# Optimization experiments

Measured on AMD Instinct MI355X. Metric: run time of the kernel, lower is better.

The kernel has to match this reference:

```python
import jax, jax.numpy as jnp
import numpy as np

N = 100000   # nodes
H = 96       # hidden_dim
A = 32       # attn_dim
De = 16      # edge_embeddings_dim
E = 500000   # edges per edge type
NEG_SLOPE = 0.01  # torch F.leaky_relu default


def setup_inputs() -> dict:
    key = jax.random.key(0)
    ks = jax.random.split(key, 24)
    nrm = lambda k, shape, s=1.0: jax.random.normal(k, shape, dtype=jnp.float32) * s
    idx = lambda k: jax.random.randint(k, (E,), 0, N, dtype=jnp.int32)
    Din = 2 * H + De
    return {
        'h': nrm(ks[0], (N, H)),
        'src0': idx(ks[1]), 'dst0': idx(ks[2]),
        'src1': idx(ks[3]), 'dst1': idx(ks[4]),
        'src2': idx(ks[5]), 'dst2': idx(ks[6]),
        'Wm0': nrm(ks[7], (Din, H), Din ** -0.5), 'bm0': jnp.zeros((H,), jnp.float32), 'ef0': nrm(ks[8], (De,)),
        'Wm1': nrm(ks[9], (Din, H), Din ** -0.5), 'bm1': jnp.zeros((H,), jnp.float32), 'ef1': nrm(ks[10], (De,)),
        'Wm2': nrm(ks[11], (Din, H), Din ** -0.5), 'bm2': jnp.zeros((H,), jnp.float32), 'ef2': nrm(ks[12], (De,)),
        'Wn0': nrm(ks[13], (H, A), H ** -0.5), 'Wa0': nrm(ks[14], (2 * A, 1), (2 * A) ** -0.5),
        'Wn1': nrm(ks[15], (H, A), H ** -0.5), 'Wa1': nrm(ks[16], (2 * A, 1), (2 * A) ** -0.5),
        'Wu': nrm(ks[17], (4 * H, H), (4 * H) ** -0.5), 'bu': jnp.zeros((H,), jnp.float32),
    }


def _leaky(x):
    return jnp.where(x > 0, x, NEG_SLOPE * x)


def _edge_msg(h, src, dst, Wm, bm, ef):
    # cat(src_h, dst_h, edge_feature) -> Linear  (dropout p=0, eval mode)
    x = jnp.concatenate([h[src], h[dst], jnp.broadcast_to(ef, (src.shape[0], ef.shape[0]))], axis=-1)
    return x @ Wm + bm  # [E, H]


def _mean_agg(m, dst):
    # fn.mean('m','msg'): per-destination mean over incoming edges
    s = jax.ops.segment_sum(m, dst, num_segments=N)
    c = jax.ops.segment_sum(jnp.ones((m.shape[0],), m.dtype), dst, num_segments=N)
    return s / jnp.maximum(c, 1.0)[:, None]


def _attn_agg(scores, m, dst):
    # per-destination softmax over mailbox (variable-size), then weighted sum
    smax = jax.ops.segment_max(scores, dst, num_segments=N)
    ex = jnp.exp(scores - smax[dst])
    den = jax.ops.segment_sum(ex, dst, num_segments=N)
    num = jax.ops.segment_sum(ex[:, None] * m, dst, num_segments=N)
    return num / jnp.maximum(den, 1e-9)[:, None]


def reference(h, src0, dst0, src1, dst1, src2, dst2,
              Wm0, bm0, ef0, Wm1, bm1, ef1, Wm2, bm2, ef2,
              Wn0, Wa0, Wn1, Wa1, Wu, bu):
    # edge type 0: intra_diff (attention), type 1: inter_diff (attention), type 2: intra_lt (mean)
    m0 = _edge_msg(h, src0, dst0, Wm0, bm0, ef0)
    m1 = _edge_msg(h, src1, dst1, Wm1, bm1, ef1)
    m2 = _edge_msg(h, src2, dst2, Wm2, bm2, ef2)

    z0 = h @ Wn0  # [N, A]
    s0 = _leaky(jnp.concatenate([z0[src0], z0[dst0]], axis=-1) @ Wa0)[:, 0]  # [E]
    z1 = h @ Wn1
    s1 = _leaky(jnp.concatenate([z1[src1], z1[dst1]], axis=-1) @ Wa1)[:, 0]

    msg0 = _attn_agg(s0, m0, dst0)   # [N, H]
    msg1 = _attn_agg(s1, m1, dst1)
    msg2 = _mean_agg(m2, dst2)

    # cross_reducer='stack' then concat over edge-type dim -> [N, 3H]
    mcat = jnp.concatenate([msg0, msg1, msg2], axis=-1)
    # cell node update: Linear(cat(h, m)) + ReLU
    return jax.nn.relu(jnp.concatenate([h, mcat], axis=-1) @ Wu + bu)
```

## Files before the change

### kernel.cpp

```cpp
#include <hip/hip_runtime.h>
#include <hip/hip_bf16.h>
#include <cstdint>

#define NN 100000
#define HH 96
#define AD 32
#define DE 16
#define EE 500000
#define NEG 0.01f

#define GSH 10
#define GSZ 1024
#define KB 98
#define CH 4096
#define BPT 123
#define PCAP 801056

typedef __bf16 bf16x8 __attribute__((ext_vector_type(8)));
typedef float  f32x4  __attribute__((ext_vector_type(4)));
typedef unsigned long long ull;
typedef unsigned long long ull2 __attribute__((ext_vector_type(2)));

__device__ __forceinline__ unsigned short f2b(float x) {
    union { float f; unsigned int u; } v; v.f = x;
    unsigned int r = v.u + 0x7fffu + ((v.u >> 16) & 1u);
    return (unsigned short)(r >> 16);
}
__device__ __forceinline__ float b2f(unsigned short h) {
    union { unsigned int u; float f; } v; v.u = ((unsigned int)h) << 16;
    return v.f;
}

__global__ void prep_kernel(const float* Wm0, const float* bm0, const float* ef0,
                            const float* Wm1, const float* bm1, const float* ef1,
                            const float* Wm2, const float* bm2, const float* ef2,
                            const float* Wn0, const float* Wa0,
                            const float* Wn1, const float* Wa1,
                            const float* Wu,
                            float* cvec, float* wvec,
                            unsigned short* BfN, unsigned short* BfU) {
    const float* Wm[3] = {Wm0, Wm1, Wm2};
    const float* bm[3] = {bm0, bm1, bm2};
    const float* ef[3] = {ef0, ef1, ef2};
    const int total = 288 + 384 + 55296 + 36864;
    for (int i = blockIdx.x * blockDim.x + threadIdx.x; i < total;
         i += gridDim.x * blockDim.x) {
        if (i < 288) {
            int t = i / 96, j = i % 96;
            float s = bm[t][j];
            for (int k = 0; k < DE; ++k) s += ef[t][k] * Wm[t][(2 * HH + k) * HH + j];
            cvec[i] = s;
        } else if (i < 288 + 384) {
            int ii = i - 288;
            int kind = ii / 96, k = ii % 96;
            const float* Wn = (kind < 2) ? Wn0 : Wn1;
            const float* Wa = (kind < 2) ? Wa0 : Wa1;
            int off = (kind & 1) ? AD : 0;
            float s = 0.f;
            for (int a = 0; a < AD; ++a) s += Wn[k * AD + a] * Wa[off + a];
            wvec[ii] = s;
        } else if (i < 288 + 384 + 55296) {
            int ii = i - 672;
            int sec = ii / 9216; int rem = ii % 9216;
            int ksc = rem / 512; int lj = rem % 512;
            int ks = ksc / 6, c = ksc % 6;
            int lane = lj / 8, jj = lj % 8;
            int quad = lane / 16, m = lane % 16;
            int k = ks * 32 + quad * 8 + jj;
            int n = c * 16 + m;
            int mt = (sec < 3) ? sec : sec - 3;
            int rowoff = (sec < 3) ? 0 : HH;
            BfN[ii] = f2b(Wm[mt][(rowoff + k) * HH + n]);
        } else {
            int ii = i - (672 + 55296);
            int ksc = ii / 512; int lj = ii % 512;
            int ks = ksc / 6, c = ksc % 6;
            int lane = lj / 8, jj = lj % 8;
            int quad = lane / 16, m = lane % 16;
            int k = ks * 32 + quad * 8 + jj;
            int n = c * 16 + m;
            BfU[ii] = f2b(Wu[k * HH + n]);
        }
    }
}

__global__ void cast_uv_kernel(const float* __restrict__ h, const float* __restrict__ wvec,
                               unsigned short* __restrict__ hb, float* __restrict__ uv) {
    int lane = threadIdx.x & 31;
    int node = (blockIdx.x * blockDim.x + threadIdx.x) >> 5;
    if (node >= NN) return;
    float h0 = h[node * HH + lane];
    float h1 = h[node * HH + 32 + lane];
    float h2 = h[node * HH + 64 + lane];
    hb[node * HH + lane] = f2b(h0);
    hb[node * HH + 32 + lane] = f2b(h1);
    hb[node * HH + 64 + lane] = f2b(h2);
    float acc[4];
#pragma unroll
    for (int q = 0; q < 4; ++q)
        acc[q] = h0 * wvec[q * 96 + lane] + h1 * wvec[q * 96 + 32 + lane] +
                 h2 * wvec[q * 96 + 64 + lane];
#pragma unroll
    for (int d = 16; d >= 1; d >>= 1)
#pragma unroll
        for (int q = 0; q < 4; ++q) acc[q] += __shfl_down(acc[q], d, 32);
    if (lane == 0) {
#pragma unroll
        for (int q = 0; q < 4; ++q) uv[q * NN + node] = acc[q];
    }
}

__global__ void zero_kernel(float4* __restrict__ p, int n4) {
    for (int i = blockIdx.x * blockDim.x + threadIdx.x; i < n4;
         i += gridDim.x * blockDim.x)
        p[i] = make_float4(0.f, 0.f, 0.f, 0.f);
}

__global__ void bucket_hist(const int* __restrict__ d0, const int* __restrict__ d1,
                            const int* __restrict__ d2, int* __restrict__ bCnt) {
    __shared__ int hist[3 * KB];
    int t = threadIdx.x;
    for (int j = t; j < 3 * KB; j += 256) hist[j] = 0;
    __syncthreads();
    const int total = 3 * EE;
    for (int i = blockIdx.x * blockDim.x + t; i < total; i += gridDim.x * blockDim.x) {
        int ty = i / EE, e = i - ty * EE;
        const int* d = (ty == 0) ? d0 : (ty == 1) ? d1 : d2;
        atomicAdd(&hist[ty * KB + (d[e] >> GSH)], 1);
    }
    __syncthreads();
    for (int j = t; j < 3 * KB; j += 256)
        if (hist[j]) atomicAdd(&bCnt[j], hist[j]);
}

__global__ void bucket_scan(const int* __restrict__ bCnt, int* __restrict__ bBase,
                            int* __restrict__ gCursor) {
    __shared__ int hist[3 * KB];
    int t = threadIdx.x;
    if (t < 3 * KB) hist[t] = bCnt[t];
    __syncthreads();
    if (t < 3) {
        int run = 0;
        for (int b = 0; b < KB; ++b) {
            bBase[t * (KB + 1) + b] = run;
            gCursor[t * KB + b] = run;
            run += hist[t * KB + b];
        }
        bBase[t * (KB + 1) + KB] = run;
    }
}

__global__ __launch_bounds__(256) void bucket_scatter(
    const int* __restrict__ s0, const int* __restrict__ d0,
    const int* __restrict__ s1, const int* __restrict__ d1,
    const int* __restrict__ s2, const int* __restrict__ d2,
    int* __restrict__ gCursor, unsigned int* __restrict__ binned) {
    __shared__ unsigned int recs[CH];
    __shared__ unsigned short rnk[CH];
    __shared__ unsigned char bkt[CH];
    __shared__ int cnt[KB];
    __shared__ int gpos[KB];
    int t = threadIdx.x;
    int type = blockIdx.x / BPT;
    int chunk = (blockIdx.x % BPT) * CH;
    const int* src = (type == 0) ? s0 : (type == 1) ? s1 : s2;
    const int* dst = (type == 0) ? d0 : (type == 1) ? d1 : d2;
    if (t < KB) cnt[t] = 0;
    __syncthreads();
#pragma unroll
    for (int k = 0; k < CH / 256; ++k) {
        int idx = k * 256 + t;
        int e = chunk + idx;
        if (e < EE) {
            int s = src[e], d = dst[e];
            int b = d >> GSH;
            recs[idx] = ((unsigned int)s << GSH) | (unsigned int)(d & (GSZ - 1));
            bkt[idx] = (unsigned char)b;
            rnk[idx] = (unsigned short)atomicAdd(&cnt[b], 1);
        } else {
            bkt[idx] = 0xFF;
        }
    }
    __syncthreads();
    if (t < KB) {
        int c = cnt[t];
        gpos[t] = (c > 0) ? atomicAdd(&gCursor[type * KB + t], c) : 0;
    }
    __syncthreads();
    unsigned int* bout = binned + (size_t)type * EE;
#pragma unroll
    for (int k = 0; k < CH / 256; ++k) {
        int idx = k * 256 + t;
        unsigned char b = bkt[idx];
        if (b != 0xFF) bout[gpos[b] + rnk[idx]] = recs[idx];
    }
}

__global__ __launch_bounds__(256) void bucket_sort(
    const unsigned int* __restrict__ binned, const int* __restrict__ bBase,
    const float* __restrict__ uv,
    ull* __restrict__ rse, ull* __restrict__ wrec) {
    __shared__ int cnt[GSZ];
    __shared__ int tsum[256];
    __shared__ float vbuf[GSZ];
    int t = threadIdx.x;
    int type = blockIdx.x / KB;
    int b = blockIdx.x % KB;
    int nodeBase = b * GSZ;
    int eb = bBase[type * (KB + 1) + b];
    int en = bBase[type * (KB + 1) + b + 1];
    int n = en - eb;
    int pbase = eb + 3 * GSZ * b;
    const unsigned int* bin = binned + (size_t)type * EE + eb;
#pragma unroll
    for (int k = 0; k < GSZ / 256; ++k) cnt[k * 256 + t] = 0;
    if (type < 2) {
        const float* vsrc = uv + (2 * type + 1) * NN;
#pragma unroll
        for (int k = 0; k < GSZ / 256; ++k) {
            int nd = nodeBase + k * 256 + t;
            vbuf[k * 256 + t] = (nd < NN) ? vsrc[nd] : 0.f;
        }
    }
    __syncthreads();
    for (int i = t; i < n; i += 256) atomicAdd(&cnt[bin[i] & (GSZ - 1)], 1);
    __syncthreads();
    int v[4], pv[4], s = 0;
#pragma unroll
    for (int k = 0; k < 4; ++k) {
        v[k] = cnt[t * 4 + k];
        pv[k] = (v[k] + 3) & ~3;
        s += pv[k];
    }
    tsum[t] = s;
    __syncthreads();
    for (int off = 1; off < 256; off <<= 1) {
        int add = (t >= off) ? tsum[t - off] : 0;
        __syncthreads();
        tsum[t] += add;
        __syncthreads();
    }
    int run = tsum[t] - s;
    int offk[4];
#pragma unroll
    for (int k = 0; k < 4; ++k) { offk[k] = run; run += pv[k]; }
    ull* wb = wrec + (size_t)type * PCAP;
#pragma unroll
    for (int k = 0; k < 4; ++k) {
        int node = nodeBase + t * 4 + k;
        if (node < NN) {
            rse[(size_t)type * NN + node] =
                ((ull)(unsigned int)pv[k] << 32) | (unsigned int)(pbase + offk[k]);
            for (int q = v[k]; q < pv[k]; ++q) wb[pbase + offk[k] + q] = 0ull;
        }
    }
    __syncthreads();
#pragma unroll
    for (int k = 0; k < 4; ++k) cnt[t * 4 + k] = offk[k];
    __syncthreads();
    const float* usrc = uv + 2 * type * NN;
    for (int i = t; i < n; i += 256) {
        unsigned int r = bin[i];
        int dl = r & (GSZ - 1);
        int p = atomicAdd(&cnt[dl], 1);
        unsigned int sidx = r >> GSH;
        float w = 1.f;
        if (type < 2) {
            float c = usrc[sidx] + vbuf[dl];
            c = fmaxf(c, NEG * c);
            w = __expf(c);
        }
        wb[pbase + p] = ((ull)__float_as_uint(w) << 32) | (ull)(sidx * 192u);
    }
}

__global__ void aggregate_kernel(const ull* __restrict__ rse,
                                 const ull* __restrict__ wrec,
                                 const unsigned short* __restrict__ hb,
                                 unsigned short* __restrict__ hagg,
                                 float* __restrict__ den) {
    const size_t NH = (size_t)NN * HH;
    int lane = threadIdx.x & 31;
    int node = (blockIdx.x * blockDim.x + threadIdx.x) >> 5;
    if (node >= NN) return;
    int t = blockIdx.y;
    ull se = rse[(size_t)t * NN + node];
    int beg = (int)(unsigned int)se;
    int end = beg + (int)(se >> 32);
    const ull* wr = wrec + (size_t)t * PCAP;
    float a0 = 0.f, a1 = 0.f, a2 = 0.f, dn = 0.f;
    const char* b0 = (const char*)hb + 4 * lane;
    const char* b1 = (const char*)hb + 128 + 2 * lane;
#define EDGE(rec)                                                              \
    {                                                                          \
        float w = __uint_as_float((unsigned int)((rec) >> 32));                \
        unsigned int off = (unsigned int)(rec);                                \
        unsigned int dv = *(const unsigned int*)(b0 + off);                    \
        unsigned int sv = *(const unsigned short*)(b1 + off);                  \
        a0 += w * __uint_as_float(dv << 16);                                   \
        a1 += w * __uint_as_float(dv & 0xFFFF0000u);                           \
        a2 += w * __uint_as_float(sv << 16);                                   \
        dn += w;                                                               \
    }
    for (int j = beg; j < end; j += 4) {
        ull2 p0 = *(const ull2*)(wr + j);
        ull2 p1 = *(const ull2*)(wr + j + 2);
        EDGE(p0[0]);
        EDGE(p0[1]);
        EDGE(p1[0]);
        EDGE(p1[1]);
    }
#undef EDGE
    float inv = (dn > 0.f) ? 1.f / dn : 0.f;
    float q0 = a0 * inv, q1 = a1 * inv, q2 = a2 * inv;
    char* mr = (char*)(hagg + (size_t)t * NH + (size_t)node * HH);
    *(unsigned int*)(mr + 4 * lane) =
        (unsigned int)f2b(q0) | ((unsigned int)f2b(q1) << 16);
    *(unsigned short*)(mr + 128 + 2 * lane) = f2b(q2);
    if (lane == 0) den[(size_t)t * NN + node] = dn;
}

__global__ __launch_bounds__(256) void msg_gemm_kernel(const unsigned short* __restrict__ hagg,
                                                       const unsigned short* __restrict__ hb,
                                                       const unsigned short* __restrict__ BfN,
                                                       const float* __restrict__ den,
                                                       const float* __restrict__ cvec,
                                                       unsigned short* __restrict__ msgb) {
    const size_t NH = (size_t)NN * HH;
    int wave = threadIdx.x >> 6;
    int lane = threadIdx.x & 63;
    int quad = lane >> 4, m = lane & 15;
    int blk = blockIdx.x * 4 + wave;
    if (blk >= NN / 16) return;
    int t = blockIdx.y;
    int r0 = blk * 16;
    const unsigned short* ha = hagg + (size_t)t * NH;
    f32x4 acc[6] = {};
#pragma unroll
    for (int ks = 0; ks < 6; ++ks) {
        const unsigned short* ap =
            (ks < 3) ? ha + (size_t)(r0 + m) * HH + ks * 32 + quad * 8
                     : hb + (size_t)(r0 + m) * HH + (ks - 3) * 32 + quad * 8;
        int sec = (ks < 3) ? t : t + 3;
        int kk = (ks < 3) ? ks : ks - 3;
        bf16x8 af = *(const bf16x8*)ap;
#pragma unroll
        for (int c = 0; c < 6; ++c) {
            bf16x8 bfv = *(const bf16x8*)(BfN + (((sec * 3 + kk) * 6 + c) << 9) + lane * 8);
            acc[c] = __builtin_amdgcn_mfma_f32_16x16x32_bf16(af, bfv, acc[c], 0, 0, 0);
        }
    }
    float dn[4];
#pragma unroll
    for (int r = 0; r < 4; ++r) dn[r] = den[(size_t)t * NN + r0 + quad * 4 + r];
#pragma unroll
    for (int c = 0; c < 6; ++c) {
        float cv = cvec[t * 96 + c * 16 + m];
#pragma unroll
        for (int r = 0; r < 4; ++r) {
            int row = r0 + quad * 4 + r;
            float val = (dn[r] > 0.f) ? (acc[c][r] + cv) : 0.f;
            msgb[(size_t)row * 288 + t * 96 + c * 16 + m] = f2b(val);
        }
    }
}

__global__ __launch_bounds__(256) void update_gemm_kernel(const unsigned short* __restrict__ hb,
                                                          const unsigned short* __restrict__ msgb,
                                                          const unsigned short* __restrict__ BfU,
                                                          const float* __restrict__ bu,
                                                          float* __restrict__ out) {
    int wave = threadIdx.x >> 6;
    int lane = threadIdx.x & 63;
    int quad = lane >> 4, m = lane & 15;
    int blk = blockIdx.x * 4 + wave;
    if (blk >= NN / 16) return;
    int r0 = blk * 16;
    f32x4 acc[6] = {};
#pragma unroll
    for (int ks = 0; ks < 12; ++ks) {
        const unsigned short* ap =
            (ks < 3) ? hb + (size_t)(r0 + m) * HH + ks * 32 + quad * 8
                     : msgb + (size_t)(r0 + m) * 288 + (ks - 3) * 32 + quad * 8;
        bf16x8 af = *(const bf16x8*)ap;
#pragma unroll
        for (int c = 0; c < 6; ++c) {
            bf16x8 bfv = *(const bf16x8*)(BfU + ((ks * 6 + c) << 9) + lane * 8);
            acc[c] = __builtin_amdgcn_mfma_f32_16x16x32_bf16(af, bfv, acc[c], 0, 0, 0);
        }
    }
#pragma unroll
    for (int c = 0; c < 6; ++c) {
        float b = bu[c * 16 + m];
#pragma unroll
        for (int r = 0; r < 4; ++r) {
            int row = r0 + quad * 4 + r;
            float v2 = acc[c][r] + b;
            out[(size_t)row * HH + c * 16 + m] = v2 > 0.f ? v2 : 0.f;
        }
    }
}

extern "C" void kernel_launch(void* const* d_in, const int* in_sizes, int n_in,
                              void* d_out, int out_size, void* d_ws, size_t ws_size,
                              hipStream_t stream) {
    (void)in_sizes; (void)n_in; (void)out_size;
    const float* h   = (const float*)d_in[0];
    const int* srcs[3] = {(const int*)d_in[1], (const int*)d_in[3], (const int*)d_in[5]};
    const int* dsts[3] = {(const int*)d_in[2], (const int*)d_in[4], (const int*)d_in[6]};
    const float* Wm0 = (const float*)d_in[7];
    const float* bm0 = (const float*)d_in[8];
    const float* ef0 = (const float*)d_in[9];
    const float* Wm1 = (const float*)d_in[10];
    const float* bm1 = (const float*)d_in[11];
    const float* ef1 = (const float*)d_in[12];
    const float* Wm2 = (const float*)d_in[13];
    const float* bm2 = (const float*)d_in[14];
    const float* ef2 = (const float*)d_in[15];
    const float* Wn0 = (const float*)d_in[16];
    const float* Wa0 = (const float*)d_in[17];
    const float* Wn1 = (const float*)d_in[18];
    const float* Wa1 = (const float*)d_in[19];
    const float* Wu  = (const float*)d_in[20];
    const float* bu  = (const float*)d_in[21];
    float* out = (float*)d_out;

    const size_t NEED = 165016320;
    if (ws_size < NEED) return;
    char* w = (char*)d_ws;
    unsigned short* msgb    = (unsigned short*)(w + 0);
    unsigned short* hb      = (unsigned short*)(w + 57600000);
    unsigned short* hagg    = (unsigned short*)(w + 76800000);
    float*          den     = (float*)(w + 134400000);
    float*          uv      = (float*)(w + 135600000);
    float*          cvec    = (float*)(w + 137200000);
    float*          wvec    = (float*)(w + 137201280);
    unsigned short* BfN     = (unsigned short*)(w + 137202816);
    unsigned short* BfU     = (unsigned short*)(w + 137313408);
    int*            bBase   = (int*)(w + 137387136);
    int*            gCursor = (int*)(w + 137388416);
    int*            bCnt    = (int*)(w + 137389696);
    ull*            rse     = (ull*)(w + 137390976);
    unsigned int*   binned  = (unsigned int*)(w + 139790976);
    ull*            wrec    = (ull*)(w + 145790976);

    prep_kernel<<<128, 256, 0, stream>>>(Wm0, bm0, ef0, Wm1, bm1, ef1, Wm2, bm2, ef2,
                                         Wn0, Wa0, Wn1, Wa1, Wu, cvec, wvec, BfN, BfU);
    cast_uv_kernel<<<12500, 256, 0, stream>>>(h, wvec, hb, uv);

    zero_kernel<<<1, 256, 0, stream>>>((float4*)bCnt, 80);
    bucket_hist<<<512, 256, 0, stream>>>(dsts[0], dsts[1], dsts[2], bCnt);
    bucket_scan<<<1, 384, 0, stream>>>(bCnt, bBase, gCursor);
    bucket_scatter<<<3 * BPT, 256, 0, stream>>>(srcs[0], dsts[0], srcs[1], dsts[1],
                                                srcs[2], dsts[2], gCursor, binned);
    bucket_sort<<<3 * KB, 256, 0, stream>>>(binned, bBase, uv, rse, wrec);

    aggregate_kernel<<<dim3(12500, 3), 256, 0, stream>>>(rse, wrec, hb, hagg, den);
    msg_gemm_kernel<<<dim3(1563, 3), 256, 0, stream>>>(hagg, hb, BfN, den, cvec, msgb);
    update_gemm_kernel<<<1563, 256, 0, stream>>>(hb, msgb, BfU, bu, out);
}
```

Baseline: 331.2 us.

## Fuse message GEMM into update GEMM via per-wave LDS staging, drop zero kernel

The per-edge-type message GEMM and the node update GEMM become one kernel. Each wave computes the 16x96 message tile for each of the three edge types, stages it in LDS as bf16, and immediately accumulates it into the update output. This removes the global msgb intermediate (about 57 MB written and read back) and one launch. The bCnt zeroing moves into prep_kernel, removing another launch. In exchange the fused kernel has fewer blocks (no grid.y over types), serial work per wave, and no barrier around the per-wave LDS use, which relies on wave-local ordering.

Result: slower. 357.6 us (+8.0%).

```diff
diff --git a/kernel.cpp b/kernel.cpp
--- a/kernel.cpp
+++ b/kernel.cpp
@@ -38,13 +38,15 @@
                             const float* Wn1, const float* Wa1,
                             const float* Wu,
                             float* cvec, float* wvec,
-                            unsigned short* BfN, unsigned short* BfU) {
+                            unsigned short* BfN, unsigned short* BfU,
+                            int* bCnt) {
     const float* Wm[3] = {Wm0, Wm1, Wm2};
     const float* bm[3] = {bm0, bm1, bm2};
     const float* ef[3] = {ef0, ef1, ef2};
+    int tid0 = blockIdx.x * blockDim.x + threadIdx.x;
+    if (tid0 < 3 * KB) bCnt[tid0] = 0;
     const int total = 288 + 384 + 55296 + 36864;
-    for (int i = blockIdx.x * blockDim.x + threadIdx.x; i < total;
-         i += gridDim.x * blockDim.x) {
+    for (int i = tid0; i < total; i += gridDim.x * blockDim.x) {
         if (i < 288) {
             int t = i / 96, j = i % 96;
             float s = bm[t][j];
@@ -110,12 +112,6 @@
     }
 }
 
-__global__ void zero_kernel(float4* __restrict__ p, int n4) {
-    for (int i = blockIdx.x * blockDim.x + threadIdx.x; i < n4;
-         i += gridDim.x * blockDim.x)
-        p[i] = make_float4(0.f, 0.f, 0.f, 0.f);
-}
-
 __global__ void bucket_hist(const int* __restrict__ d0, const int* __restrict__ d1,
                             const int* __restrict__ d2, int* __restrict__ bCnt) {
     __shared__ int hist[3 * KB];
@@ -320,73 +316,74 @@
     if (lane == 0) den[(size_t)t * NN + node] = dn;
 }
 
-__global__ __launch_bounds__(256) void msg_gemm_kernel(const unsigned short* __restrict__ hagg,
-                                                       const unsigned short* __restrict__ hb,
-                                                       const unsigned short* __restrict__ BfN,
-                                                       const float* __restrict__ den,
-                                                       const float* __restrict__ cvec,
-                                                       unsigned short* __restrict__ msgb) {
+__global__ __launch_bounds__(256) void fused_gemm_kernel(
+    const unsigned short* __restrict__ hagg,
+    const unsigned short* __restrict__ hb,
+    const unsigned short* __restrict__ BfN,
+    const unsigned short* __restrict__ BfU,
+    const float* __restrict__ den,
+    const float* __restrict__ cvec,
+    const float* __restrict__ bu,
+    float* __restrict__ out) {
     const size_t NH = (size_t)NN * HH;
-    int wave = threadIdx.x >> 6;
-    int lane = threadIdx.x & 63;
-    int quad = lane >> 4, m = lane & 15;
-    int blk = blockIdx.x * 4 + wave;
-    if (blk >= NN / 16) return;
-    int t = blockIdx.y;
-    int r0 = blk * 16;
-    const unsigned short* ha = hagg + (size_t)t * NH;
-    f32x4 acc[6] = {};
-#pragma unroll
-    for (int ks = 0; ks < 6; ++ks) {
-        const unsigned short* ap =
-            (ks < 3) ? ha + (size_t)(r0 + m) * HH + ks * 32 + quad * 8
-                     : hb + (size_t)(r0 + m) * HH + (ks - 3) * 32 + quad * 8;
-        int sec = (ks < 3) ? t : t + 3;
-        int kk = (ks < 3) ? ks : ks - 3;
-        bf16x8 af = *(const bf16x8*)ap;
-#pragma unroll
-        for (int c = 0; c < 6; ++c) {
-            bf16x8 bfv = *(const bf16x8*)(BfN + (((sec * 3 + kk) * 6 + c) << 9) + lane * 8);
-            acc[c] = __builtin_amdgcn_mfma_f32_16x16x32_bf16(af, bfv, acc[c], 0, 0, 0);
-        }
-    }
-    float dn[4];
-#pragma unroll
-    for (int r = 0; r < 4; ++r) dn[r] = den[(size_t)t * NN + r0 + quad * 4 + r];
-#pragma unroll
-    for (int c = 0; c < 6; ++c) {
-        float cv = cvec[t * 96 + c * 16 + m];
-#pragma unroll
-        for (int r = 0; r < 4; ++r) {
-            int row = r0 + quad * 4 + r;
-            float val = (dn[r] > 0.f) ? (acc[c][r] + cv) : 0.f;
-            msgb[(size_t)row * 288 + t * 96 + c * 16 + m] = f2b(val);
-        }
-    }
-}
-
-__global__ __launch_bounds__(256) void update_gemm_kernel(const unsigned short* __restrict__ hb,
-                                                          const unsigned short* __restrict__ msgb,
-                                                          const unsigned short* __restrict__ BfU,
-                                                          const float* __restrict__ bu,
-                                                          float* __restrict__ out) {
+    __shared__ unsigned short lds[4][16][104];
     int wave = threadIdx.x >> 6;
     int lane = threadIdx.x & 63;
     int quad = lane >> 4, m = lane & 15;
     int blk = blockIdx.x * 4 + wave;
     if (blk >= NN / 16) return;
     int r0 = blk * 16;
-    f32x4 acc[6] = {};
-#pragma unroll
-    for (int ks = 0; ks < 12; ++ks) {
-        const unsigned short* ap =
-            (ks < 3) ? hb + (size_t)(r0 + m) * HH + ks * 32 + quad * 8
-                     : msgb + (size_t)(r0 + m) * 288 + (ks - 3) * 32 + quad * 8;
-        bf16x8 af = *(const bf16x8*)ap;
+    unsigned short (*L)[104] = lds[wave];
+
+    f32x4 accO[6] = {};
+#pragma unroll
+    for (int ks = 0; ks < 3; ++ks) {
+        bf16x8 af = *(const bf16x8*)(hb + (size_t)(r0 + m) * HH + ks * 32 + quad * 8);
 #pragma unroll
         for (int c = 0; c < 6; ++c) {
             bf16x8 bfv = *(const bf16x8*)(BfU + ((ks * 6 + c) << 9) + lane * 8);
-            acc[c] = __builtin_amdgcn_mfma_f32_16x16x32_bf16(af, bfv, acc[c], 0, 0, 0);
+            accO[c] = __builtin_amdgcn_mfma_f32_16x16x32_bf16(af, bfv, accO[c], 0, 0, 0);
+        }
+    }
+#pragma unroll 1
+    for (int t = 0; t < 3; ++t) {
+        const unsigned short* ha = hagg + (size_t)t * NH;
+        f32x4 acc[6] = {};
+#pragma unroll
+        for (int ks = 0; ks < 6; ++ks) {
+            const unsigned short* ap =
+                (ks < 3) ? ha + (size_t)(r0 + m) * HH + ks * 32 + quad * 8
+                         : hb + (size_t)(r0 + m) * HH + (ks - 3) * 32 + quad * 8;
+            int sec = (ks < 3) ? t : t + 3;
+            int kk = (ks < 3) ? ks : ks - 3;
+            bf16x8 af = *(const bf16x8*)ap;
+#pragma unroll
+            for (int c = 0; c < 6; ++c) {
+                bf16x8 bfv = *(const bf16x8*)(BfN + (((sec * 3 + kk) * 6 + c) << 9) + lane * 8);
+                acc[c] = __builtin_amdgcn_mfma_f32_16x16x32_bf16(af, bfv, acc[c], 0, 0, 0);
+            }
+        }
+        float dn[4];
+#pragma unroll
+        for (int r = 0; r < 4; ++r) dn[r] = den[(size_t)t * NN + r0 + quad * 4 + r];
+#pragma unroll
+        for (int c = 0; c < 6; ++c) {
+            float cv = cvec[t * 96 + c * 16 + m];
+#pragma unroll
+            for (int r = 0; r < 4; ++r) {
+                float val = (dn[r] > 0.f) ? (acc[c][r] + cv) : 0.f;
+                L[quad * 4 + r][c * 16 + m] = f2b(val);
+            }
+        }
+#pragma unroll
+        for (int ks = 0; ks < 3; ++ks) {
+            bf16x8 af = *(const bf16x8*)&L[m][ks * 32 + quad * 8];
+            int ku = 3 + t * 3 + ks;
+#pragma unroll
+            for (int c = 0; c < 6; ++c) {
+                bf16x8 bfv = *(const bf16x8*)(BfU + ((ku * 6 + c) << 9) + lane * 8);
+                accO[c] = __builtin_amdgcn_mfma_f32_16x16x32_bf16(af, bfv, accO[c], 0, 0, 0);
+            }
         }
     }
 #pragma unroll
@@ -395,7 +392,7 @@
 #pragma unroll
         for (int r = 0; r < 4; ++r) {
             int row = r0 + quad * 4 + r;
-            float v2 = acc[c][r] + b;
+            float v2 = accO[c][r] + b;
             out[(size_t)row * HH + c * 16 + m] = v2 > 0.f ? v2 : 0.f;
         }
     }
@@ -428,7 +425,6 @@
     const size_t NEED = 165016320;
     if (ws_size < NEED) return;
     char* w = (char*)d_ws;
-    unsigned short* msgb    = (unsigned short*)(w + 0);
     unsigned short* hb      = (unsigned short*)(w + 57600000);
     unsigned short* hagg    = (unsigned short*)(w + 76800000);
     float*          den     = (float*)(w + 134400000);
@@ -445,10 +441,10 @@
     ull*            wrec    = (ull*)(w + 145790976);
 
     prep_kernel<<<128, 256, 0, stream>>>(Wm0, bm0, ef0, Wm1, bm1, ef1, Wm2, bm2, ef2,
-                                         Wn0, Wa0, Wn1, Wa1, Wu, cvec, wvec, BfN, BfU);
+                                         Wn0, Wa0, Wn1, Wa1, Wu, cvec, wvec, BfN, BfU,
+                                         bCnt);
     cast_uv_kernel<<<12500, 256, 0, stream>>>(h, wvec, hb, uv);
 
-    zero_kernel<<<1, 256, 0, stream>>>((float4*)bCnt, 80);
     bucket_hist<<<512, 256, 0, stream>>>(dsts[0], dsts[1], dsts[2], bCnt);
     bucket_scan<<<1, 384, 0, stream>>>(bCnt, bBase, gCursor);
     bucket_scatter<<<3 * BPT, 256, 0, stream>>>(srcs[0], dsts[0], srcs[1], dsts[1],
@@ -456,6 +452,5 @@
     bucket_sort<<<3 * KB, 256, 0, stream>>>(binned, bBase, uv, rse, wrec);
 
     aggregate_kernel<<<dim3(12500, 3), 256, 0, stream>>>(rse, wrec, hb, hagg, den);
-    msg_gemm_kernel<<<dim3(1563, 3), 256, 0, stream>>>(hagg, hb, BfN, den, cvec, msgb);
-    update_gemm_kernel<<<1563, 256, 0, stream>>>(hb, msgb, BfU, bu, out);
-}
+    fused_gemm_kernel<<<1563, 256, 0, stream>>>(hagg, hb, BfN, BfU, den, cvec, bu, out);
+}
```

## Fuse edge aggregation with message GEMM via LDS and fold bucket zeroing into prep

Applied to the files above, without the earlier changes.

Aggregation and the per-type message GEMM now run in one kernel. Each 512-thread block aggregates 16 nodes into shared memory, then six waves each compute one 16-column output tile with MFMA. This avoids writing and re-reading the aggregated hidden buffer and the denominator array in global memory, and removes one launch. The bucket-count zeroing moves into prep_kernel, removing zero_kernel. In exchange, only 6 of the 8 waves do the GEMM phase, a block-wide barrier is added, and each block's GEMM waits on its slowest aggregation group.

Result: no change. 336.1 us (+1.5%).

```diff
diff --git a/kernel.cpp b/kernel.cpp
--- a/kernel.cpp
+++ b/kernel.cpp
@@ -38,13 +38,15 @@
                             const float* Wn1, const float* Wa1,
                             const float* Wu,
                             float* cvec, float* wvec,
-                            unsigned short* BfN, unsigned short* BfU) {
+                            unsigned short* BfN, unsigned short* BfU,
+                            int* bCnt) {
     const float* Wm[3] = {Wm0, Wm1, Wm2};
     const float* bm[3] = {bm0, bm1, bm2};
     const float* ef[3] = {ef0, ef1, ef2};
+    int tid0 = blockIdx.x * blockDim.x + threadIdx.x;
+    if (tid0 < 3 * KB) bCnt[tid0] = 0;
     const int total = 288 + 384 + 55296 + 36864;
-    for (int i = blockIdx.x * blockDim.x + threadIdx.x; i < total;
-         i += gridDim.x * blockDim.x) {
+    for (int i = tid0; i < total; i += gridDim.x * blockDim.x) {
         if (i < 288) {
             int t = i / 96, j = i % 96;
             float s = bm[t][j];
@@ -110,12 +112,6 @@
     }
 }
 
-__global__ void zero_kernel(float4* __restrict__ p, int n4) {
-    for (int i = blockIdx.x * blockDim.x + threadIdx.x; i < n4;
-         i += gridDim.x * blockDim.x)
-        p[i] = make_float4(0.f, 0.f, 0.f, 0.f);
-}
-
 __global__ void bucket_hist(const int* __restrict__ d0, const int* __restrict__ d1,
                             const int* __restrict__ d2, int* __restrict__ bCnt) {
     __shared__ int hist[3 * KB];
@@ -274,16 +270,21 @@
     }
 }
 
-__global__ void aggregate_kernel(const ull* __restrict__ rse,
-                                 const ull* __restrict__ wrec,
-                                 const unsigned short* __restrict__ hb,
-                                 unsigned short* __restrict__ hagg,
-                                 float* __restrict__ den) {
-    const size_t NH = (size_t)NN * HH;
-    int lane = threadIdx.x & 31;
-    int node = (blockIdx.x * blockDim.x + threadIdx.x) >> 5;
-    if (node >= NN) return;
+__global__ __launch_bounds__(512) void agg_msg_kernel(
+    const ull* __restrict__ rse,
+    const ull* __restrict__ wrec,
+    const unsigned short* __restrict__ hb,
+    const unsigned short* __restrict__ BfN,
+    const float* __restrict__ cvec,
+    unsigned short* __restrict__ msgb) {
+    __shared__ unsigned short Lh[16][104];
+    __shared__ float dnL[16];
     int t = blockIdx.y;
+    int tid = threadIdx.x;
+    int lane = tid & 31;
+    int g = tid >> 5;
+    int node = blockIdx.x * 16 + g;
+
     ull se = rse[(size_t)t * NN + node];
     int beg = (int)(unsigned int)se;
     int end = beg + (int)(se >> 32);
@@ -313,55 +314,39 @@
 #undef EDGE
     float inv = (dn > 0.f) ? 1.f / dn : 0.f;
     float q0 = a0 * inv, q1 = a1 * inv, q2 = a2 * inv;
-    char* mr = (char*)(hagg + (size_t)t * NH + (size_t)node * HH);
+    char* mr = (char*)&Lh[g][0];
     *(unsigned int*)(mr + 4 * lane) =
         (unsigned int)f2b(q0) | ((unsigned int)f2b(q1) << 16);
     *(unsigned short*)(mr + 128 + 2 * lane) = f2b(q2);
-    if (lane == 0) den[(size_t)t * NN + node] = dn;
-}
-
-__global__ __launch_bounds__(256) void msg_gemm_kernel(const unsigned short* __restrict__ hagg,
-                                                       const unsigned short* __restrict__ hb,
-                                                       const unsigned short* __restrict__ BfN,
-                                                       const float* __restrict__ den,
-                                                       const float* __restrict__ cvec,
-                                                       unsigned short* __restrict__ msgb) {
-    const size_t NH = (size_t)NN * HH;
-    int wave = threadIdx.x >> 6;
-    int lane = threadIdx.x & 63;
-    int quad = lane >> 4, m = lane & 15;
-    int blk = blockIdx.x * 4 + wave;
-    if (blk >= NN / 16) return;
-    int t = blockIdx.y;
-    int r0 = blk * 16;
-    const unsigned short* ha = hagg + (size_t)t * NH;
-    f32x4 acc[6] = {};
+    if (lane == 0) dnL[g] = dn;
+    __syncthreads();
+
+    int wave = tid >> 6;
+    if (wave >= 6) return;
+    int l64 = tid & 63;
+    int quad = l64 >> 4, m = l64 & 15;
+    int c = wave;
+    int r0 = blockIdx.x * 16;
+    f32x4 acc = {};
 #pragma unroll
     for (int ks = 0; ks < 6; ++ks) {
-        const unsigned short* ap =
-            (ks < 3) ? ha + (size_t)(r0 + m) * HH + ks * 32 + quad * 8
-                     : hb + (size_t)(r0 + m) * HH + (ks - 3) * 32 + quad * 8;
+        bf16x8 af;
+        if (ks < 3)
+            af = *(const bf16x8*)((const char*)&Lh[m][0] + ks * 64 + quad * 16);
+        else
+            af = *(const bf16x8*)(hb + (size_t)(r0 + m) * HH + (ks - 3) * 32 + quad * 8);
         int sec = (ks < 3) ? t : t + 3;
         int kk = (ks < 3) ? ks : ks - 3;
-        bf16x8 af = *(const bf16x8*)ap;
-#pragma unroll
-        for (int c = 0; c < 6; ++c) {
-            bf16x8 bfv = *(const bf16x8*)(BfN + (((sec * 3 + kk) * 6 + c) << 9) + lane * 8);
-            acc[c] = __builtin_amdgcn_mfma_f32_16x16x32_bf16(af, bfv, acc[c], 0, 0, 0);
-        }
-    }
-    float dn[4];
-#pragma unroll
-    for (int r = 0; r < 4; ++r) dn[r] = den[(size_t)t * NN + r0 + quad * 4 + r];
-#pragma unroll
-    for (int c = 0; c < 6; ++c) {
-        float cv = cvec[t * 96 + c * 16 + m];
-#pragma unroll
-        for (int r = 0; r < 4; ++r) {
-            int row = r0 + quad * 4 + r;
-            float val = (dn[r] > 0.f) ? (acc[c][r] + cv) : 0.f;
-            msgb[(size_t)row * 288 + t * 96 + c * 16 + m] = f2b(val);
-        }
+        bf16x8 bfv = *(const bf16x8*)(BfN + (((sec * 3 + kk) * 6 + c) << 9) + l64 * 8);
+        acc = __builtin_amdgcn_mfma_f32_16x16x32_bf16(af, bfv, acc, 0, 0, 0);
+    }
+    float cv = cvec[t * 96 + c * 16 + m];
+#pragma unroll
+    for (int r = 0; r < 4; ++r) {
+        int row = r0 + quad * 4 + r;
+        float dnv = dnL[quad * 4 + r];
+        float val = (dnv > 0.f) ? (acc[r] + cv) : 0.f;
+        msgb[(size_t)row * 288 + t * 96 + c * 16 + m] = f2b(val);
     }
 }
 
@@ -430,8 +415,6 @@
     char* w = (char*)d_ws;
     unsigned short* msgb    = (unsigned short*)(w + 0);
     unsigned short* hb      = (unsigned short*)(w + 57600000);
-    unsigned short* hagg    = (unsigned short*)(w + 76800000);
-    float*          den     = (float*)(w + 134400000);
     float*          uv      = (float*)(w + 135600000);
     float*          cvec    = (float*)(w + 137200000);
     float*          wvec    = (float*)(w + 137201280);
@@ -445,17 +428,16 @@
     ull*            wrec    = (ull*)(w + 145790976);
 
     prep_kernel<<<128, 256, 0, stream>>>(Wm0, bm0, ef0, Wm1, bm1, ef1, Wm2, bm2, ef2,
-                                         Wn0, Wa0, Wn1, Wa1, Wu, cvec, wvec, BfN, BfU);
+                                         Wn0, Wa0, Wn1, Wa1, Wu, cvec, wvec, BfN, BfU,
+                                         bCnt);
     cast_uv_kernel<<<12500, 256, 0, stream>>>(h, wvec, hb, uv);
 
-    zero_kernel<<<1, 256, 0, stream>>>((float4*)bCnt, 80);
     bucket_hist<<<512, 256, 0, stream>>>(dsts[0], dsts[1], dsts[2], bCnt);
     bucket_scan<<<1, 384, 0, stream>>>(bCnt, bBase, gCursor);
     bucket_scatter<<<3 * BPT, 256, 0, stream>>>(srcs[0], dsts[0], srcs[1], dsts[1],
                                                 srcs[2], dsts[2], gCursor, binned);
     bucket_sort<<<3 * KB, 256, 0, stream>>>(binned, bBase, uv, rse, wrec);
 
-    aggregate_kernel<<<dim3(12500, 3), 256, 0, stream>>>(rse, wrec, hb, hagg, den);
-    msg_gemm_kernel<<<dim3(1563, 3), 256, 0, stream>>>(hagg, hb, BfN, den, cvec, msgb);
+    agg_msg_kernel<<<dim3(6250, 3), 512, 0, stream>>>(rse, wrec, hb, BfN, cvec, msgb);
     update_gemm_kernel<<<1563, 256, 0, stream>>>(hb, msgb, BfU, bu, out);
 }
```

## Halve sort bucket size, use wave-shuffle scan, fold counter zeroing into prep

Applied to the files above, without the earlier changes.

Node buckets for the destination sort shrink from 1024 to 512 nodes, doubling the number of bucket_sort blocks to spread the work over more CUs and cut per-block shared-memory work. The block-wide Hillis-Steele scan with many __syncthreads is replaced by a 64-wide wave shuffle scan plus a small cross-wave sum. The separate zero_kernel launch is removed by zeroing the bucket counters inside prep_kernel. The trade-offs are more buckets to count and scatter, a wider bucket_scan launch, and more padding per bucket in the PCAP-sized record buffer.

Result: no change. 328.9 us (-0.7%).

```diff
diff --git a/kernel.cpp b/kernel.cpp
--- a/kernel.cpp
+++ b/kernel.cpp
@@ -9,11 +9,11 @@
 #define EE 500000
 #define NEG 0.01f
 
-#define GSH 10
-#define GSZ 1024
-#define KB 98
-#define CH 4096
-#define BPT 123
+#define GSH 9
+#define GSZ 512
+#define KB 196
+#define CH 2048
+#define BPT 245
 #define PCAP 801056
 
 typedef __bf16 bf16x8 __attribute__((ext_vector_type(8)));
@@ -38,13 +38,15 @@
                             const float* Wn1, const float* Wa1,
                             const float* Wu,
                             float* cvec, float* wvec,
-                            unsigned short* BfN, unsigned short* BfU) {
+                            unsigned short* BfN, unsigned short* BfU,
+                            int* bCnt) {
     const float* Wm[3] = {Wm0, Wm1, Wm2};
     const float* bm[3] = {bm0, bm1, bm2};
     const float* ef[3] = {ef0, ef1, ef2};
+    int tid0 = blockIdx.x * blockDim.x + threadIdx.x;
+    if (tid0 < 3 * KB) bCnt[tid0] = 0;
     const int total = 288 + 384 + 55296 + 36864;
-    for (int i = blockIdx.x * blockDim.x + threadIdx.x; i < total;
-         i += gridDim.x * blockDim.x) {
+    for (int i = tid0; i < total; i += gridDim.x * blockDim.x) {
         if (i < 288) {
             int t = i / 96, j = i % 96;
             float s = bm[t][j];
@@ -110,12 +112,6 @@
     }
 }
 
-__global__ void zero_kernel(float4* __restrict__ p, int n4) {
-    for (int i = blockIdx.x * blockDim.x + threadIdx.x; i < n4;
-         i += gridDim.x * blockDim.x)
-        p[i] = make_float4(0.f, 0.f, 0.f, 0.f);
-}
-
 __global__ void bucket_hist(const int* __restrict__ d0, const int* __restrict__ d1,
                             const int* __restrict__ d2, int* __restrict__ bCnt) {
     __shared__ int hist[3 * KB];
@@ -201,8 +197,8 @@
     const float* __restrict__ uv,
     ull* __restrict__ rse, ull* __restrict__ wrec) {
     __shared__ int cnt[GSZ];
-    __shared__ int tsum[256];
     __shared__ float vbuf[GSZ];
+    __shared__ int wsum[4];
     int t = threadIdx.x;
     int type = blockIdx.x / KB;
     int b = blockIdx.x % KB;
@@ -212,51 +208,49 @@
     int n = en - eb;
     int pbase = eb + 3 * GSZ * b;
     const unsigned int* bin = binned + (size_t)type * EE + eb;
-#pragma unroll
-    for (int k = 0; k < GSZ / 256; ++k) cnt[k * 256 + t] = 0;
+    cnt[t] = 0;
+    cnt[t + 256] = 0;
     if (type < 2) {
         const float* vsrc = uv + (2 * type + 1) * NN;
-#pragma unroll
-        for (int k = 0; k < GSZ / 256; ++k) {
-            int nd = nodeBase + k * 256 + t;
-            vbuf[k * 256 + t] = (nd < NN) ? vsrc[nd] : 0.f;
-        }
+        int nd0 = nodeBase + t, nd1 = nodeBase + 256 + t;
+        vbuf[t] = (nd0 < NN) ? vsrc[nd0] : 0.f;
+        vbuf[t + 256] = (nd1 < NN) ? vsrc[nd1] : 0.f;
     }
     __syncthreads();
     for (int i = t; i < n; i += 256) atomicAdd(&cnt[bin[i] & (GSZ - 1)], 1);
     __syncthreads();
-    int v[4], pv[4], s = 0;
-#pragma unroll
-    for (int k = 0; k < 4; ++k) {
-        v[k] = cnt[t * 4 + k];
-        pv[k] = (v[k] + 3) & ~3;
-        s += pv[k];
-    }
-    tsum[t] = s;
-    __syncthreads();
-    for (int off = 1; off < 256; off <<= 1) {
-        int add = (t >= off) ? tsum[t - off] : 0;
-        __syncthreads();
-        tsum[t] += add;
-        __syncthreads();
-    }
-    int run = tsum[t] - s;
-    int offk[4];
-#pragma unroll
-    for (int k = 0; k < 4; ++k) { offk[k] = run; run += pv[k]; }
+    int v0 = cnt[t * 2], v1 = cnt[t * 2 + 1];
+    int p0 = (v0 + 3) & ~3, p1 = (v1 + 3) & ~3;
+    int s = p0 + p1;
+    int lane = t & 63, wv = t >> 6;
+    int val = s;
+#pragma unroll
+    for (int d = 1; d < 64; d <<= 1) {
+        int o = __shfl_up(val, d, 64);
+        if (lane >= d) val += o;
+    }
+    if (lane == 63) wsum[wv] = val;
+    __syncthreads();
+    int wpre = 0;
+#pragma unroll
+    for (int i = 0; i < 4; ++i) wpre += (i < wv) ? wsum[i] : 0;
+    int excl = val - s + wpre;
+    int off0 = excl, off1 = excl + p0;
     ull* wb = wrec + (size_t)type * PCAP;
-#pragma unroll
-    for (int k = 0; k < 4; ++k) {
-        int node = nodeBase + t * 4 + k;
-        if (node < NN) {
-            rse[(size_t)type * NN + node] =
-                ((ull)(unsigned int)pv[k] << 32) | (unsigned int)(pbase + offk[k]);
-            for (int q = v[k]; q < pv[k]; ++q) wb[pbase + offk[k] + q] = 0ull;
-        }
-    }
-    __syncthreads();
-#pragma unroll
-    for (int k = 0; k < 4; ++k) cnt[t * 4 + k] = offk[k];
+    int node0 = nodeBase + t * 2, node1 = nodeBase + t * 2 + 1;
+    if (node0 < NN) {
+        rse[(size_t)type * NN + node0] =
+            ((ull)(unsigned int)p0 << 32) | (unsigned int)(pbase + off0);
+        for (int q = v0; q < p0; ++q) wb[pbase + off0 + q] = 0ull;
+    }
+    if (node1 < NN) {
+        rse[(size_t)type * NN + node1] =
+            ((ull)(unsigned int)p1 << 32) | (unsigned int)(pbase + off1);
+        for (int q = v1; q < p1; ++q) wb[pbase + off1 + q] = 0ull;
+    }
+    __syncthreads();
+    cnt[t * 2] = off0;
+    cnt[t * 2 + 1] = off1;
     __syncthreads();
     const float* usrc = uv + 2 * type * NN;
     for (int i = t; i < n; i += 256) {
@@ -425,7 +419,7 @@
     const float* bu  = (const float*)d_in[21];
     float* out = (float*)d_out;
 
-    const size_t NEED = 165016320;
+    const size_t NEED = 165019776;
     if (ws_size < NEED) return;
     char* w = (char*)d_ws;
     unsigned short* msgb    = (unsigned short*)(w + 0);
@@ -438,19 +432,19 @@
     unsigned short* BfN     = (unsigned short*)(w + 137202816);
     unsigned short* BfU     = (unsigned short*)(w + 137313408);
     int*            bBase   = (int*)(w + 137387136);
-    int*            gCursor = (int*)(w + 137388416);
-    int*            bCnt    = (int*)(w + 137389696);
-    ull*            rse     = (ull*)(w + 137390976);
-    unsigned int*   binned  = (unsigned int*)(w + 139790976);
-    ull*            wrec    = (ull*)(w + 145790976);
+    int*            gCursor = (int*)(w + 137389568);
+    int*            bCnt    = (int*)(w + 137392000);
+    ull*            rse     = (ull*)(w + 137394432);
+    unsigned int*   binned  = (unsigned int*)(w + 139794432);
+    ull*            wrec    = (ull*)(w + 145794432);
 
     prep_kernel<<<128, 256, 0, stream>>>(Wm0, bm0, ef0, Wm1, bm1, ef1, Wm2, bm2, ef2,
-                                         Wn0, Wa0, Wn1, Wa1, Wu, cvec, wvec, BfN, BfU);
+                                         Wn0, Wa0, Wn1, Wa1, Wu, cvec, wvec, BfN, BfU,
+                                         bCnt);
     cast_uv_kernel<<<12500, 256, 0, stream>>>(h, wvec, hb, uv);
 
-    zero_kernel<<<1, 256, 0, stream>>>((float4*)bCnt, 80);
     bucket_hist<<<512, 256, 0, stream>>>(dsts[0], dsts[1], dsts[2], bCnt);
-    bucket_scan<<<1, 384, 0, stream>>>(bCnt, bBase, gCursor);
+    bucket_scan<<<1, 640, 0, stream>>>(bCnt, bBase, gCursor);
     bucket_scatter<<<3 * BPT, 256, 0, stream>>>(srcs[0], dsts[0], srcs[1], dsts[1],
                                                 srcs[2], dsts[2], gCursor, binned);
     bucket_sort<<<3 * KB, 256, 0, stream>>>(binned, bBase, uv, rse, wrec);
```
